# Performance work log

Hardware: AMD Instinct MI355X
Metric: run time of the kernel (lower is better)

The kernel has to match this reference:

```python
import jax, jax.numpy as jnp
import numpy as np

D_IN = 768
D_H = 256
N_CTX = 4

def setup_inputs() -> dict:
    key = jax.random.key(0)
    ks = jax.random.split(key, 6)
    b, s = 64, 2048
    return {
        "last_hidden_states": jax.random.normal(ks[0], (b, s, D_IN), dtype=jnp.float32),
        "W1": jax.random.normal(ks[1], (D_IN, D_H), dtype=jnp.float32) / np.sqrt(D_IN),
        "b1": jnp.zeros((D_H,), dtype=jnp.float32),
        "context_vector": jax.random.normal(ks[2], (D_H, N_CTX), dtype=jnp.float32),
        "W2": jax.random.normal(ks[3], (N_CTX * D_IN, D_IN), dtype=jnp.float32) / np.sqrt(N_CTX * D_IN),
        "b2": jnp.zeros((D_IN,), dtype=jnp.float32),
    }

def reference(last_hidden_states, W1, b1, context_vector, W2, b2):
    b = last_hidden_states.shape[0]
    # h: [b, s, 256]
    h = jnp.tanh(jnp.einsum('bsd,dh->bsh', last_hidden_states, W1) + b1)
    # scores over sequence dim for each of 4 context vectors: [b, s, 4]
    scores = jax.nn.softmax(jnp.einsum('bsh,hc->bsc', h, context_vector), axis=1)
    # weighted sums: [b, 4, 768] -> flatten to [b, 3072]
    pooled = jnp.einsum('bsc,bsd->bcd', scores, last_hidden_states).reshape(b, -1)
    pooled = jax.nn.relu(pooled)
    return pooled @ W2 + b2
```

## Files before the change

kernel.cpp:

```cpp
#include <hip/hip_runtime.h>

typedef _Float16 f16x8 __attribute__((ext_vector_type(8)));
typedef float f32x4 __attribute__((ext_vector_type(4)));

#define D_IN 768
#define D_H  256
#define SEQ  2048

__global__ __launch_bounds__(256) void k0_w1t(const float* __restrict__ W1,
                                              _Float16* __restrict__ W1T) {
  __shared__ float tl[64][65];
  const int kb = blockIdx.x, nb = blockIdx.y, t = threadIdx.x;
#pragma unroll
  for (int rep = 0; rep < 16; ++rep) {
    const int row = rep * 4 + (t >> 6), col = t & 63;
    tl[row][col] = W1[(size_t)(kb * 64 + row) * D_H + nb * 64 + col];
  }
  __syncthreads();
#pragma unroll
  for (int rep = 0; rep < 16; ++rep) {
    const int n = rep * 4 + (t >> 6), k = t & 63;
    W1T[(size_t)(nb * 64 + n) * D_IN + kb * 64 + k] = (_Float16)tl[k][n];
  }
}

__global__ __launch_bounds__(512) void k1_logits(const float* __restrict__ X,
    const _Float16* __restrict__ W1T, const float* __restrict__ b1,
    const float* __restrict__ C, float* __restrict__ logits) {
  __shared__ _Float16 Al[128][72];
  __shared__ _Float16 Bl[256][72];
  __shared__ float red[4][32][4];
  const int t = threadIdx.x;
  const int M0 = blockIdx.x * 128;

  const int arow = t >> 2, akc = t & 3;
  const int bcol = t >> 1, bko = (t & 1) * 32;
  const float*    Ag = X + (size_t)(M0 + arow) * D_IN + akc * 8;
  const _Float16* Bg = W1T + (size_t)bcol * D_IN + bko;

  f32x4 acc[2][8];
#pragma unroll
  for (int i = 0; i < 2; ++i)
#pragma unroll
    for (int j = 0; j < 8; ++j) acc[i][j] = f32x4{0.f, 0.f, 0.f, 0.f};

  float4 a0 = *(const float4*)(Ag);
  float4 a1 = *(const float4*)(Ag + 4);
  float4 a2 = *(const float4*)(Ag + 32);
  float4 a3 = *(const float4*)(Ag + 36);
  uint4 bb0 = *(const uint4*)(Bg);
  uint4 bb1 = *(const uint4*)(Bg + 8);
  uint4 bb2 = *(const uint4*)(Bg + 16);
  uint4 bb3 = *(const uint4*)(Bg + 24);

  const int lane = t & 63, wv = t >> 6;
  const int wm = wv >> 1, wn = wv & 1;
  const int l15 = lane & 15, kg = lane >> 4;

  for (int kt = 0; kt < 12; ++kt) {
    f16x8 ha, hb;
    ha[0] = (_Float16)a0.x; ha[1] = (_Float16)a0.y; ha[2] = (_Float16)a0.z; ha[3] = (_Float16)a0.w;
    ha[4] = (_Float16)a1.x; ha[5] = (_Float16)a1.y; ha[6] = (_Float16)a1.z; ha[7] = (_Float16)a1.w;
    hb[0] = (_Float16)a2.x; hb[1] = (_Float16)a2.y; hb[2] = (_Float16)a2.z; hb[3] = (_Float16)a2.w;
    hb[4] = (_Float16)a3.x; hb[5] = (_Float16)a3.y; hb[6] = (_Float16)a3.z; hb[7] = (_Float16)a3.w;
    *(f16x8*)&Al[arow][akc * 8]      = ha;
    *(f16x8*)&Al[arow][akc * 8 + 32] = hb;
    *(uint4*)&Bl[bcol][bko]      = bb0;
    *(uint4*)&Bl[bcol][bko + 8]  = bb1;
    *(uint4*)&Bl[bcol][bko + 16] = bb2;
    *(uint4*)&Bl[bcol][bko + 24] = bb3;
    __syncthreads();
    if (kt < 11) {
      const float* An = Ag + (kt + 1) * 64;
      a0 = *(const float4*)(An);
      a1 = *(const float4*)(An + 4);
      a2 = *(const float4*)(An + 32);
      a3 = *(const float4*)(An + 36);
      const _Float16* Bn = Bg + (kt + 1) * 64;
      bb0 = *(const uint4*)(Bn);
      bb1 = *(const uint4*)(Bn + 8);
      bb2 = *(const uint4*)(Bn + 16);
      bb3 = *(const uint4*)(Bn + 24);
    }
#pragma unroll
    for (int st = 0; st < 2; ++st) {
      f16x8 af[2], bf[8];
#pragma unroll
      for (int i = 0; i < 2; ++i)
        af[i] = *(const f16x8*)&Al[wm * 32 + i * 16 + l15][kg * 8 + st * 32];
#pragma unroll
      for (int j = 0; j < 8; ++j)
        bf[j] = *(const f16x8*)&Bl[wn * 128 + j * 16 + l15][kg * 8 + st * 32];
#pragma unroll
      for (int j = 0; j < 8; ++j)
#pragma unroll
        for (int i = 0; i < 2; ++i)
          acc[i][j] = __builtin_amdgcn_mfma_f32_16x16x32_f16(af[i], bf[j], acc[i][j], 0, 0, 0);
    }
    __syncthreads();
  }

  ((float*)red)[t] = 0.f;
  __syncthreads();

  float part[2][4][4];
#pragma unroll
  for (int i = 0; i < 2; ++i)
#pragma unroll
    for (int r = 0; r < 4; ++r)
#pragma unroll
      for (int c = 0; c < 4; ++c) part[i][r][c] = 0.f;

#pragma unroll
  for (int j = 0; j < 8; ++j) {
    const int col = wn * 128 + j * 16 + l15;
    const float4 c4 = *(const float4*)(C + col * 4);
    const float bv = b1[col];
#pragma unroll
    for (int i = 0; i < 2; ++i)
#pragma unroll
      for (int r = 0; r < 4; ++r) {
        float z = acc[i][j][r] + bv;
        z = fminf(fmaxf(z, -15.f), 15.f);
        const float e = __expf(2.f * z);
        const float h = (e - 1.f) / (e + 1.f);
        part[i][r][0] += h * c4.x;
        part[i][r][1] += h * c4.y;
        part[i][r][2] += h * c4.z;
        part[i][r][3] += h * c4.w;
      }
  }
#pragma unroll
  for (int off = 1; off < 16; off <<= 1) {
#pragma unroll
    for (int i = 0; i < 2; ++i)
#pragma unroll
      for (int r = 0; r < 4; ++r)
#pragma unroll
        for (int c = 0; c < 4; ++c)
          part[i][r][c] += __shfl_xor(part[i][r][c], off, 64);
  }
  if (l15 == 0) {
#pragma unroll
    for (int i = 0; i < 2; ++i)
#pragma unroll
      for (int r = 0; r < 4; ++r)
#pragma unroll
        for (int c = 0; c < 4; ++c)
          atomicAdd(&red[wm][i * 16 + kg * 4 + r][c], part[i][r][c]);
  }
  __syncthreads();
  {
    const int wmx = t >> 7, row = (t >> 2) & 31, c = t & 3;
    const int m = M0 + wmx * 32 + row;
    const int b = m >> 11, s = m & 2047;
    logits[((size_t)(b * 4 + c)) * SEQ + s] = red[wmx][row][c];
  }
}

__global__ __launch_bounds__(256) void k2_softmax(const float* __restrict__ logits,
                                                  float* __restrict__ scores) {
  const int b = blockIdx.x, t = threadIdx.x;
  const int lane = t & 63, wv = t >> 6;
  __shared__ float rmax[4][4], rsum[4][4];
  float lv[4][8];
#pragma unroll
  for (int c = 0; c < 4; ++c)
#pragma unroll
    for (int j = 0; j < 8; ++j)
      lv[c][j] = logits[((size_t)(b * 4 + c)) * SEQ + j * 256 + t];
#pragma unroll
  for (int c = 0; c < 4; ++c) {
    float m = lv[c][0];
#pragma unroll
    for (int j = 1; j < 8; ++j) m = fmaxf(m, lv[c][j]);
#pragma unroll
    for (int off = 1; off < 64; off <<= 1) m = fmaxf(m, __shfl_xor(m, off, 64));
    if (lane == 0) rmax[wv][c] = m;
  }
  __syncthreads();
  float mx[4], inv[4];
#pragma unroll
  for (int c = 0; c < 4; ++c)
    mx[c] = fmaxf(fmaxf(rmax[0][c], rmax[1][c]), fmaxf(rmax[2][c], rmax[3][c]));
#pragma unroll
  for (int c = 0; c < 4; ++c) {
    float ssum = 0.f;
#pragma unroll
    for (int j = 0; j < 8; ++j) { lv[c][j] = __expf(lv[c][j] - mx[c]); ssum += lv[c][j]; }
#pragma unroll
    for (int off = 1; off < 64; off <<= 1) ssum += __shfl_xor(ssum, off, 64);
    if (lane == 0) rsum[wv][c] = ssum;
  }
  __syncthreads();
#pragma unroll
  for (int c = 0; c < 4; ++c)
    inv[c] = 1.f / (rsum[0][c] + rsum[1][c] + rsum[2][c] + rsum[3][c]);
#pragma unroll
  for (int j = 0; j < 8; ++j) {
    float4 o;
    o.x = lv[0][j] * inv[0]; o.y = lv[1][j] * inv[1];
    o.z = lv[2][j] * inv[2]; o.w = lv[3][j] * inv[3];
    *(float4*)&scores[((size_t)b * SEQ + j * 256 + t) * 4] = o;
  }
}

__global__ __launch_bounds__(256) void k3_pool(const float* __restrict__ X,
                                               const float* __restrict__ scores,
                                               float* __restrict__ pooled) {
  const int chunk = blockIdx.x, b = blockIdx.y, t = threadIdx.x;
  const int s0 = t >> 5, d4 = t & 31;
  const float* Xb = X + (size_t)b * SEQ * D_IN + chunk * 128 + d4 * 4;
  const float* Sb = scores + (size_t)b * SEQ * 4;
  float acc[4][4];
#pragma unroll
  for (int c = 0; c < 4; ++c)
#pragma unroll
    for (int j = 0; j < 4; ++j) acc[c][j] = 0.f;
#pragma unroll 2
  for (int s = s0; s < SEQ; s += 8) {
    const float4 w = *(const float4*)(Sb + (size_t)s * 4);
    const float4 x = *(const float4*)(Xb + (size_t)s * D_IN);
    const float wc[4] = {w.x, w.y, w.z, w.w};
    const float xv[4] = {x.x, x.y, x.z, x.w};
#pragma unroll
    for (int c = 0; c < 4; ++c)
#pragma unroll
      for (int j = 0; j < 4; ++j) acc[c][j] += wc[c] * xv[j];
  }
  __shared__ float r3[8][32][16];
#pragma unroll
  for (int c = 0; c < 4; ++c)
#pragma unroll
    for (int j = 0; j < 4; ++j) r3[s0][d4][c * 4 + j] = acc[c][j];
  __syncthreads();
#pragma unroll
  for (int o = t; o < 512; o += 256) {
    const int dd = o >> 4, cj = o & 15, c = cj >> 2, j = cj & 3;
    float v = 0.f;
#pragma unroll
    for (int p = 0; p < 8; ++p) v += r3[p][dd][cj];
    v = fmaxf(v, 0.f);
    pooled[(size_t)b * 3072 + c * D_IN + chunk * 128 + dd * 4 + j] = v;
  }
}

__global__ __launch_bounds__(256) void k4_partial(const float* __restrict__ pooled,
                                                  const float* __restrict__ W2,
                                                  float* __restrict__ partial) {
  const int jc = blockIdx.x, kc = blockIdx.y, t = threadIdx.x;
  __shared__ float plds[64 * 192];
  __shared__ float sum2[64][64];
  for (int idx = t; idx < 64 * 192; idx += 256) {
    const int b = idx / 192, k = idx - b * 192;
    plds[idx] = pooled[(size_t)b * 3072 + kc * 192 + k];
  }
  __syncthreads();
  const int j = t & 63, kp = t >> 6;
  float acc[64];
#pragma unroll
  for (int b = 0; b < 64; ++b) acc[b] = 0.f;
  const float* W2p = W2 + (size_t)(kc * 192 + kp * 48) * D_IN + jc * 64 + j;
  const float* pb = plds + kp * 48;
  for (int ki = 0; ki < 48; ki += 4) {
    const float w0 = W2p[(size_t)(ki + 0) * D_IN];
    const float w1 = W2p[(size_t)(ki + 1) * D_IN];
    const float w2 = W2p[(size_t)(ki + 2) * D_IN];
    const float w3 = W2p[(size_t)(ki + 3) * D_IN];
#pragma unroll
    for (int b = 0; b < 64; ++b) {
      const float4 p4 = *(const float4*)(pb + b * 192 + ki);
      acc[b] += p4.x * w0 + p4.y * w1 + p4.z * w2 + p4.w * w3;
    }
  }
#pragma unroll
  for (int p = 0; p < 4; ++p) {
    if (kp == p) {
      if (p == 0) {
#pragma unroll
        for (int b = 0; b < 64; ++b) sum2[b][j] = acc[b];
      } else {
#pragma unroll
        for (int b = 0; b < 64; ++b) sum2[b][j] += acc[b];
      }
    }
    __syncthreads();
  }
  for (int idx = t; idx < 4096; idx += 256) {
    const int b = idx >> 6, jj = idx & 63;
    partial[(size_t)kc * 49152 + (size_t)b * D_IN + jc * 64 + jj] = sum2[b][jj];
  }
}

__global__ __launch_bounds__(256) void k5_final(const float* __restrict__ partial,
                                                const float* __restrict__ b2,
                                                float* __restrict__ out) {
  const int o = blockIdx.x * 256 + threadIdx.x;
  float v = b2[o % D_IN];
#pragma unroll
  for (int p = 0; p < 16; ++p) v += partial[(size_t)p * 49152 + o];
  out[o] = v;
}

extern "C" void kernel_launch(void* const* d_in, const int* in_sizes, int n_in,
                              void* d_out, int out_size, void* d_ws, size_t ws_size,
                              hipStream_t stream) {
  const float* X  = (const float*)d_in[0];
  const float* W1 = (const float*)d_in[1];
  const float* b1 = (const float*)d_in[2];
  const float* C  = (const float*)d_in[3];
  const float* W2 = (const float*)d_in[4];
  const float* b2 = (const float*)d_in[5];
  float* out = (float*)d_out;
  char* ws = (char*)d_ws;
  _Float16* W1T  = (_Float16*)ws;
  float* logits  = (float*)(ws + 393216);
  float* scores  = (float*)(ws + 2490368);
  float* pooled  = (float*)(ws + 4587520);
  float* partial = (float*)(ws + 5373952);

  k0_w1t   <<<dim3(12, 4), 256, 0, stream>>>(W1, W1T);
  k1_logits<<<1024,        512, 0, stream>>>(X, W1T, b1, C, logits);
  k2_softmax<<<64,         256, 0, stream>>>(logits, scores);
  k3_pool  <<<dim3(6, 64), 256, 0, stream>>>(X, scores, pooled);
  k4_partial<<<dim3(12,16),256, 0, stream>>>(pooled, W2, partial);
  k5_final <<<192,         256, 0, stream>>>(partial, b2, out);
}
```

Before: 285.4 us.

## Fuse logits, local softmax and pooling into one kernel keeping X tile in LDS

Each block now loads a 64-row tile of X once, converts it to fp16 and keeps it in shared memory. The block computes the tanh logits with MFMA, then a block-local softmax (max and sum), and writes partial weighted sums of X plus its stats. A small combine kernel rescales the partials online-softmax style to form the pooled vectors. This removes the second full pass over X and the logits/scores round trips, at the cost of large LDS use, low occupancy and fp16 partial sums.

```diff
diff --git a/kernel.cpp b/kernel.cpp
--- a/kernel.cpp
+++ b/kernel.cpp
@@ -24,75 +24,71 @@
   }
 }
 
-__global__ __launch_bounds__(512) void k1_logits(const float* __restrict__ X,
+__global__ __launch_bounds__(512, 1) void kf_fused(const float* __restrict__ X,
     const _Float16* __restrict__ W1T, const float* __restrict__ b1,
-    const float* __restrict__ C, float* __restrict__ logits) {
-  __shared__ _Float16 Al[128][72];
+    const float* __restrict__ C, _Float16* __restrict__ Ppart,
+    float* __restrict__ stats) {
+  __shared__ _Float16 Xl[64][776];
   __shared__ _Float16 Bl[256][72];
-  __shared__ float red[4][32][4];
+  __shared__ float red[64][4];
+  __shared__ float ms4[4], Ss4[4];
   const int t = threadIdx.x;
-  const int M0 = blockIdx.x * 128;
-
-  const int arow = t >> 2, akc = t & 3;
-  const int bcol = t >> 1, bko = (t & 1) * 32;
-  const float*    Ag = X + (size_t)(M0 + arow) * D_IN + akc * 8;
-  const _Float16* Bg = W1T + (size_t)bcol * D_IN + bko;
-
-  f32x4 acc[2][8];
+  const int bid = blockIdx.x;
+  const size_t M0 = (size_t)bid * 64;
+
+  const int xrow = t >> 3, xkc = t & 7;
+  const int bcolS = t >> 1, bh = t & 1;
+  const float*    Ag = X + (M0 + xrow) * D_IN + xkc * 8;
+  const _Float16* Bg = W1T + (size_t)bcolS * D_IN + bh * 32;
+
+  f32x4 acc[2][4];
 #pragma unroll
   for (int i = 0; i < 2; ++i)
 #pragma unroll
-    for (int j = 0; j < 8; ++j) acc[i][j] = f32x4{0.f, 0.f, 0.f, 0.f};
+    for (int j = 0; j < 4; ++j) acc[i][j] = f32x4{0.f, 0.f, 0.f, 0.f};
 
   float4 a0 = *(const float4*)(Ag);
   float4 a1 = *(const float4*)(Ag + 4);
-  float4 a2 = *(const float4*)(Ag + 32);
-  float4 a3 = *(const float4*)(Ag + 36);
-  uint4 bb0 = *(const uint4*)(Bg);
-  uint4 bb1 = *(const uint4*)(Bg + 8);
-  uint4 bb2 = *(const uint4*)(Bg + 16);
-  uint4 bb3 = *(const uint4*)(Bg + 24);
+  uint4 bq0 = *(const uint4*)(Bg);
+  uint4 bq1 = *(const uint4*)(Bg + 8);
+  uint4 bq2 = *(const uint4*)(Bg + 16);
+  uint4 bq3 = *(const uint4*)(Bg + 24);
 
   const int lane = t & 63, wv = t >> 6;
-  const int wm = wv >> 1, wn = wv & 1;
+  const int wm = wv >> 2, wn = wv & 3;
   const int l15 = lane & 15, kg = lane >> 4;
 
   for (int kt = 0; kt < 12; ++kt) {
-    f16x8 ha, hb;
+    f16x8 ha;
     ha[0] = (_Float16)a0.x; ha[1] = (_Float16)a0.y; ha[2] = (_Float16)a0.z; ha[3] = (_Float16)a0.w;
     ha[4] = (_Float16)a1.x; ha[5] = (_Float16)a1.y; ha[6] = (_Float16)a1.z; ha[7] = (_Float16)a1.w;
-    hb[0] = (_Float16)a2.x; hb[1] = (_Float16)a2.y; hb[2] = (_Float16)a2.z; hb[3] = (_Float16)a2.w;
-    hb[4] = (_Float16)a3.x; hb[5] = (_Float16)a3.y; hb[6] = (_Float16)a3.z; hb[7] = (_Float16)a3.w;
-    *(f16x8*)&Al[arow][akc * 8]      = ha;
-    *(f16x8*)&Al[arow][akc * 8 + 32] = hb;
-    *(uint4*)&Bl[bcol][bko]      = bb0;
-    *(uint4*)&Bl[bcol][bko + 8]  = bb1;
-    *(uint4*)&Bl[bcol][bko + 16] = bb2;
-    *(uint4*)&Bl[bcol][bko + 24] = bb3;
+    *(f16x8*)&Xl[xrow][kt * 64 + xkc * 8] = ha;
+    *(uint4*)&Bl[bcolS][bh * 32]      = bq0;
+    *(uint4*)&Bl[bcolS][bh * 32 + 8]  = bq1;
+    *(uint4*)&Bl[bcolS][bh * 32 + 16] = bq2;
+    *(uint4*)&Bl[bcolS][bh * 32 + 24] = bq3;
     __syncthreads();
     if (kt < 11) {
       const float* An = Ag + (kt + 1) * 64;
       a0 = *(const float4*)(An);
       a1 = *(const float4*)(An + 4);
-      a2 = *(const float4*)(An + 32);
-      a3 = *(const float4*)(An + 36);
       const _Float16* Bn = Bg + (kt + 1) * 64;
-      bb0 = *(const uint4*)(Bn);
-      bb1 = *(const uint4*)(Bn + 8);
-      bb2 = *(const uint4*)(Bn + 16);
-      bb3 = *(const uint4*)(Bn + 24);
+      bq0 = *(const uint4*)(Bn);
+      bq1 = *(const uint4*)(Bn + 8);
+      bq2 = *(const uint4*)(Bn + 16);
+      bq3 = *(const uint4*)(Bn + 24);
     }
 #pragma unroll
     for (int st = 0; st < 2; ++st) {
-      f16x8 af[2], bf[8];
+      f16x8 af[2], bf[4];
 #pragma unroll
       for (int i = 0; i < 2; ++i)
-        af[i] = *(const f16x8*)&Al[wm * 32 + i * 16 + l15][kg * 8 + st * 32];
-#pragma unroll
-      for (int j = 0; j < 8; ++j)
-        bf[j] = *(const f16x8*)&Bl[wn * 128 + j * 16 + l15][kg * 8 + st * 32];
-#pragma unroll
-      for (int j = 0; j < 8; ++j)
+        af[i] = *(const f16x8*)&Xl[wm * 32 + i * 16 + l15][kt * 64 + st * 32 + kg * 8];
+#pragma unroll
+      for (int j = 0; j < 4; ++j)
+        bf[j] = *(const f16x8*)&Bl[wn * 64 + j * 16 + l15][st * 32 + kg * 8];
+#pragma unroll
+      for (int j = 0; j < 4; ++j)
 #pragma unroll
         for (int i = 0; i < 2; ++i)
           acc[i][j] = __builtin_amdgcn_mfma_f32_16x16x32_f16(af[i], bf[j], acc[i][j], 0, 0, 0);
@@ -100,7 +96,7 @@
     __syncthreads();
   }
 
-  ((float*)red)[t] = 0.f;
+  if (t < 256) ((float*)red)[t] = 0.f;
   __syncthreads();
 
   float part[2][4][4];
@@ -112,8 +108,8 @@
       for (int c = 0; c < 4; ++c) part[i][r][c] = 0.f;
 
 #pragma unroll
-  for (int j = 0; j < 8; ++j) {
-    const int col = wn * 128 + j * 16 + l15;
+  for (int j = 0; j < 4; ++j) {
+    const int col = wn * 64 + j * 16 + l15;
     const float4 c4 = *(const float4*)(C + col * 4);
     const float bv = b1[col];
 #pragma unroll
@@ -147,101 +143,84 @@
       for (int r = 0; r < 4; ++r)
 #pragma unroll
         for (int c = 0; c < 4; ++c)
-          atomicAdd(&red[wm][i * 16 + kg * 4 + r][c], part[i][r][c]);
-  }
-  __syncthreads();
-  {
-    const int wmx = t >> 7, row = (t >> 2) & 31, c = t & 3;
-    const int m = M0 + wmx * 32 + row;
-    const int b = m >> 11, s = m & 2047;
-    logits[((size_t)(b * 4 + c)) * SEQ + s] = red[wmx][row][c];
-  }
-}
-
-__global__ __launch_bounds__(256) void k2_softmax(const float* __restrict__ logits,
-                                                  float* __restrict__ scores) {
+          atomicAdd(&red[wm * 32 + i * 16 + kg * 4 + r][c], part[i][r][c]);
+  }
+  __syncthreads();
+
+  if (t < 4) {
+    float m = red[0][t];
+#pragma unroll 8
+    for (int r = 1; r < 64; ++r) m = fmaxf(m, red[r][t]);
+    ms4[t] = m;
+  }
+  __syncthreads();
+  if (t < 256) {
+    const int r = t >> 2, c = t & 3;
+    red[r][c] = __expf(red[r][c] - ms4[c]);
+  }
+  __syncthreads();
+  if (t < 4) {
+    float s = 0.f;
+#pragma unroll 8
+    for (int r = 0; r < 64; ++r) s += red[r][t];
+    Ss4[t] = s;
+  }
+  __syncthreads();
+  if (t < 8) stats[(size_t)bid * 8 + t] = (t & 1) ? Ss4[t >> 1] : ms4[t >> 1];
+
+  const int pc = t >> 7, pch = t & 127;
+  if (pch < 96) {
+    float a8[8] = {0.f, 0.f, 0.f, 0.f, 0.f, 0.f, 0.f, 0.f};
+    for (int r = 0; r < 64; ++r) {
+      const float w = red[r][pc];
+      const f16x8 x8 = *(const f16x8*)&Xl[r][pch * 8];
+#pragma unroll
+      for (int k = 0; k < 8; ++k) a8[k] += w * (float)x8[k];
+    }
+    f16x8 o;
+#pragma unroll
+    for (int k = 0; k < 8; ++k) o[k] = (_Float16)a8[k];
+    *(f16x8*)&Ppart[(size_t)bid * 3072 + pc * 768 + pch * 8] = o;
+  }
+}
+
+__global__ __launch_bounds__(256) void kc_combine(const _Float16* __restrict__ Ppart,
+    const float* __restrict__ stats, float* __restrict__ pooled) {
   const int b = blockIdx.x, t = threadIdx.x;
-  const int lane = t & 63, wv = t >> 6;
-  __shared__ float rmax[4][4], rsum[4][4];
-  float lv[4][8];
-#pragma unroll
-  for (int c = 0; c < 4; ++c)
-#pragma unroll
-    for (int j = 0; j < 8; ++j)
-      lv[c][j] = logits[((size_t)(b * 4 + c)) * SEQ + j * 256 + t];
+  __shared__ float sm[32][8];
+  __shared__ float Mc[4], Dc[4], fw[32][4];
+  sm[t >> 3][t & 7] = stats[((size_t)b * 32 + (t >> 3)) * 8 + (t & 7)];
+  __syncthreads();
+  if (t < 4) {
+    float m = sm[0][t * 2];
+#pragma unroll
+    for (int blk = 1; blk < 32; ++blk) m = fmaxf(m, sm[blk][t * 2]);
+    Mc[t] = m;
+  }
+  __syncthreads();
+  if (t < 128) {
+    const int blk = t >> 2, c = t & 3;
+    fw[blk][c] = __expf(sm[blk][c * 2] - Mc[c]);
+  }
+  __syncthreads();
+  if (t < 4) {
+    float s = 0.f;
+#pragma unroll
+    for (int blk = 0; blk < 32; ++blk) s += fw[blk][t] * sm[blk][t * 2 + 1];
+    Dc[t] = 1.f / s;
+  }
+  __syncthreads();
 #pragma unroll
   for (int c = 0; c < 4; ++c) {
-    float m = lv[c][0];
-#pragma unroll
-    for (int j = 1; j < 8; ++j) m = fmaxf(m, lv[c][j]);
-#pragma unroll
-    for (int off = 1; off < 64; off <<= 1) m = fmaxf(m, __shfl_xor(m, off, 64));
-    if (lane == 0) rmax[wv][c] = m;
-  }
-  __syncthreads();
-  float mx[4], inv[4];
-#pragma unroll
-  for (int c = 0; c < 4; ++c)
-    mx[c] = fmaxf(fmaxf(rmax[0][c], rmax[1][c]), fmaxf(rmax[2][c], rmax[3][c]));
-#pragma unroll
-  for (int c = 0; c < 4; ++c) {
-    float ssum = 0.f;
-#pragma unroll
-    for (int j = 0; j < 8; ++j) { lv[c][j] = __expf(lv[c][j] - mx[c]); ssum += lv[c][j]; }
-#pragma unroll
-    for (int off = 1; off < 64; off <<= 1) ssum += __shfl_xor(ssum, off, 64);
-    if (lane == 0) rsum[wv][c] = ssum;
-  }
-  __syncthreads();
-#pragma unroll
-  for (int c = 0; c < 4; ++c)
-    inv[c] = 1.f / (rsum[0][c] + rsum[1][c] + rsum[2][c] + rsum[3][c]);
-#pragma unroll
-  for (int j = 0; j < 8; ++j) {
-    float4 o;
-    o.x = lv[0][j] * inv[0]; o.y = lv[1][j] * inv[1];
-    o.z = lv[2][j] * inv[2]; o.w = lv[3][j] * inv[3];
-    *(float4*)&scores[((size_t)b * SEQ + j * 256 + t) * 4] = o;
-  }
-}
-
-__global__ __launch_bounds__(256) void k3_pool(const float* __restrict__ X,
-                                               const float* __restrict__ scores,
-                                               float* __restrict__ pooled) {
-  const int chunk = blockIdx.x, b = blockIdx.y, t = threadIdx.x;
-  const int s0 = t >> 5, d4 = t & 31;
-  const float* Xb = X + (size_t)b * SEQ * D_IN + chunk * 128 + d4 * 4;
-  const float* Sb = scores + (size_t)b * SEQ * 4;
-  float acc[4][4];
-#pragma unroll
-  for (int c = 0; c < 4; ++c)
-#pragma unroll
-    for (int j = 0; j < 4; ++j) acc[c][j] = 0.f;
-#pragma unroll 2
-  for (int s = s0; s < SEQ; s += 8) {
-    const float4 w = *(const float4*)(Sb + (size_t)s * 4);
-    const float4 x = *(const float4*)(Xb + (size_t)s * D_IN);
-    const float wc[4] = {w.x, w.y, w.z, w.w};
-    const float xv[4] = {x.x, x.y, x.z, x.w};
-#pragma unroll
-    for (int c = 0; c < 4; ++c)
-#pragma unroll
-      for (int j = 0; j < 4; ++j) acc[c][j] += wc[c] * xv[j];
-  }
-  __shared__ float r3[8][32][16];
-#pragma unroll
-  for (int c = 0; c < 4; ++c)
-#pragma unroll
-    for (int j = 0; j < 4; ++j) r3[s0][d4][c * 4 + j] = acc[c][j];
-  __syncthreads();
-#pragma unroll
-  for (int o = t; o < 512; o += 256) {
-    const int dd = o >> 4, cj = o & 15, c = cj >> 2, j = cj & 3;
-    float v = 0.f;
-#pragma unroll
-    for (int p = 0; p < 8; ++p) v += r3[p][dd][cj];
-    v = fmaxf(v, 0.f);
-    pooled[(size_t)b * 3072 + c * D_IN + chunk * 128 + dd * 4 + j] = v;
+#pragma unroll
+    for (int rep = 0; rep < 3; ++rep) {
+      const int d = rep * 256 + t;
+      float acc = 0.f;
+#pragma unroll 4
+      for (int blk = 0; blk < 32; ++blk)
+        acc += fw[blk][c] * (float)Ppart[((size_t)(b * 32 + blk)) * 3072 + c * 768 + d];
+      pooled[(size_t)b * 3072 + c * 768 + d] = fmaxf(acc * Dc[c], 0.f);
+    }
   }
 }
 
@@ -313,16 +292,15 @@
   const float* b2 = (const float*)d_in[5];
   float* out = (float*)d_out;
   char* ws = (char*)d_ws;
-  _Float16* W1T  = (_Float16*)ws;
-  float* logits  = (float*)(ws + 393216);
-  float* scores  = (float*)(ws + 2490368);
-  float* pooled  = (float*)(ws + 4587520);
-  float* partial = (float*)(ws + 5373952);
-
-  k0_w1t   <<<dim3(12, 4), 256, 0, stream>>>(W1, W1T);
-  k1_logits<<<1024,        512, 0, stream>>>(X, W1T, b1, C, logits);
-  k2_softmax<<<64,         256, 0, stream>>>(logits, scores);
-  k3_pool  <<<dim3(6, 64), 256, 0, stream>>>(X, scores, pooled);
-  k4_partial<<<dim3(12,16),256, 0, stream>>>(pooled, W2, partial);
-  k5_final <<<192,         256, 0, stream>>>(partial, b2, out);
-}
+  _Float16* W1T   = (_Float16*)ws;
+  float* pooled   = (float*)(ws + 393216);
+  float* stats    = (float*)(ws + 1179648);
+  _Float16* Ppart = (_Float16*)(ws + 1245184);
+  float* partial  = (float*)(ws + 1245184);
+
+  k0_w1t    <<<dim3(12, 4), 256, 0, stream>>>(W1, W1T);
+  kf_fused  <<<2048,        512, 0, stream>>>(X, W1T, b1, C, Ppart, stats);
+  kc_combine<<<64,          256, 0, stream>>>(Ppart, stats, pooled);
+  k4_partial<<<dim3(12,16), 256, 0, stream>>>(pooled, W2, partial);
+  k5_final  <<<192,         256, 0, stream>>>(partial, b2, out);
+}
```

New measurement: 365.4 us. 1.28x slower.
